# Kernel optimization log

Measured on AMD Instinct MI355X. Metric: run time of the kernel, lower is better.

## Reference

```python
import jax, jax.numpy as jnp
import numpy as np

N_NODES = 100000
N_EDGES = 1600000
NEG_SLOPE = 0.2  # PyG GATConv default


def _glorot(key, shape):
    fan = sum(shape[:2]) if len(shape) > 1 else shape[0] * 2
    s = jnp.sqrt(6.0 / fan)
    return jax.random.uniform(key, shape, jnp.float32, -s, s)


def gat_layer(x, src, dst, edge_attr, W, a_src, a_dst, We, a_e, b, heads, out_ch, concat):
    """Faithful PyG GATConv (add_self_loops=True, fill_value='mean', edge_dim set)."""
    n = x.shape[0]
    # self-loop edge_attr = mean of incoming edge_attr per dst node (0 if none)
    deg = jax.ops.segment_sum(jnp.ones((src.shape[0],), edge_attr.dtype), dst, num_segments=n)
    loop_attr = jax.ops.segment_sum(edge_attr, dst, num_segments=n) / jnp.maximum(deg, 1.0)[:, None]
    loop = jnp.arange(n, dtype=src.dtype)
    src_f = jnp.concatenate([src, loop])
    dst_f = jnp.concatenate([dst, loop])
    ea = jnp.concatenate([edge_attr, loop_attr], axis=0)
    # node transform -> [n, H, C]
    h = (x @ W).reshape(n, heads, out_ch)
    al_src = jnp.sum(h * a_src, axis=-1)  # [n, H]
    al_dst = jnp.sum(h * a_dst, axis=-1)  # [n, H]
    e = (ea @ We).reshape(-1, heads, out_ch)
    al_e = jnp.sum(e * a_e, axis=-1)      # [Ef, H]
    alpha = jax.nn.leaky_relu(al_src[src_f] + al_dst[dst_f] + al_e, negative_slope=NEG_SLOPE)
    # segment softmax over destination nodes (every node has a self loop)
    m = jax.ops.segment_max(alpha, dst_f, num_segments=n)
    ex = jnp.exp(alpha - m[dst_f])
    den = jax.ops.segment_sum(ex, dst_f, num_segments=n)
    att = ex / den[dst_f]                 # [Ef, H]
    out = jax.ops.segment_sum(att[:, :, None] * h[src_f], dst_f, num_segments=n)  # [n, H, C]
    out = out.reshape(n, heads * out_ch) if concat else out.mean(axis=1)
    return out + b


def setup_inputs() -> dict:
    key = jax.random.key(0)
    ks = jax.random.split(key, 20)
    x = jax.random.normal(ks[0], (N_NODES, 5), jnp.float32)
    edge_index = jax.random.randint(ks[1], (2, N_EDGES), 0, N_NODES, jnp.int64)
    edge_attr = jax.random.normal(ks[2], (N_EDGES, 2), jnp.float32)
    # conv1: in=5, out=32, heads=4, concat -> 128
    p = {
        "W1": _glorot(ks[3], (5, 128)), "aS1": _glorot(ks[4], (4, 32)),
        "aD1": _glorot(ks[5], (4, 32)), "We1": _glorot(ks[6], (2, 128)),
        "aE1": _glorot(ks[7], (4, 32)), "b1": jnp.zeros((128,), jnp.float32),
        # conv2: in=128, out=32, heads=2, concat -> 64
        "W2": _glorot(ks[8], (128, 64)), "aS2": _glorot(ks[9], (2, 32)),
        "aD2": _glorot(ks[10], (2, 32)), "We2": _glorot(ks[11], (2, 64)),
        "aE2": _glorot(ks[12], (2, 32)), "b2": jnp.zeros((64,), jnp.float32),
        # conv3: in=64, out=1, heads=1, concat=False
        "W3": _glorot(ks[13], (64, 1)), "aS3": _glorot(ks[14], (1, 1)),
        "aD3": _glorot(ks[15], (1, 1)), "We3": _glorot(ks[16], (2, 1)),
        "aE3": _glorot(ks[17], (1, 1)), "b3": jnp.zeros((1,), jnp.float32),
    }
    return {"x": x, "edge_index": edge_index, "edge_attr": edge_attr, **p}


def reference(x, edge_index, edge_attr,
              W1, aS1, aD1, We1, aE1, b1,
              W2, aS2, aD2, We2, aE2, b2,
              W3, aS3, aD3, We3, aE3, b3):
    src, dst = edge_index[0], edge_index[1]
    h = gat_layer(x, src, dst, edge_attr, W1, aS1, aD1, We1, aE1, b1, 4, 32, True)
    h = jax.nn.elu(h)  # dropout is identity in eval
    h = gat_layer(h, src, dst, edge_attr, W2, aS2, aD2, We2, aE2, b2, 2, 32, True)
    h = jax.nn.elu(h)
    h = gat_layer(h, src, dst, edge_attr, W3, aS3, aD3, We3, aE3, b3, 1, 1, False)
    return jax.nn.sigmoid(h).squeeze(-1)  # [N]
```

## Files before the change

### kernel.cpp

```cpp
#include <hip/hip_runtime.h>
#include <math.h>

#define NN 100000
#define NE 1600000
#define NPB 256
#define NPB_SHIFT 8
#define NB ((NN + NPB - 1) / NPB)
#define NCHUNK 512
#define CH ((NE + NCHUNK - 1) / NCHUNK)
#define LOG2E 1.44269504088896f

__device__ __forceinline__ float lrelu(float x) { return fmaxf(x, 0.2f * x); }
__device__ __forceinline__ float elu1(float x) { return x > 0.f ? x : (__expf(x) - 1.f); }
__device__ __forceinline__ float fexp2(float x) {
#if __has_builtin(__builtin_amdgcn_exp2f)
    return __builtin_amdgcn_exp2f(x);
#else
    return exp2f(x);
#endif
}
__device__ __forceinline__ unsigned bf16rne(float f) {
    unsigned u = __float_as_uint(f);
    return (u + 0x7FFFu + ((u >> 16) & 1u)) >> 16;
}
__device__ __forceinline__ float bf16lo(unsigned u) { return __uint_as_float(u << 16); }
__device__ __forceinline__ float bf16hi(unsigned u) {
    return __uint_as_float(u & 0xFFFF0000u);
}

__global__ void __launch_bounds__(256) k_binA0(const int* __restrict__ dst,
                                               int* __restrict__ bucket_cnt) {
    __shared__ int hist[NB];
    int t = threadIdx.x;
    for (int b = t; b < NB; b += 256) hist[b] = 0;
    __syncthreads();
    int c0 = blockIdx.x * CH, c1 = min(NE, c0 + CH);
    for (int e = c0 + t; e < c1; e += 256) atomicAdd(&hist[dst[e] >> NPB_SHIFT], 1);
    __syncthreads();
    for (int b = t; b < NB; b += 256)
        if (hist[b]) atomicAdd(&bucket_cnt[b], hist[b]);
}

__global__ void __launch_bounds__(512) k_bscan(const int* __restrict__ bucket_cnt,
                                               int* __restrict__ bucket_base,
                                               int* __restrict__ bucket_tail) {
    __shared__ int s[512];
    int t = threadIdx.x;
    int v = (t < NB) ? bucket_cnt[t] : 0;
    s[t] = v;
    __syncthreads();
    for (int off = 1; off < 512; off <<= 1) {
        int x = (t >= off) ? s[t - off] : 0;
        __syncthreads();
        if (t >= off) s[t] += x;
        __syncthreads();
    }
    if (t < NB) {
        int ex = s[t] - v;
        bucket_base[t] = ex;
        bucket_tail[t] = ex;
        if (t == NB - 1) bucket_base[NB] = s[t];
    }
}

__global__ void __launch_bounds__(256) k_binA2(const int* __restrict__ src,
                                               const int* __restrict__ dst,
                                               const float* __restrict__ ea,
                                               int* __restrict__ bucket_tail,
                                               uint2* __restrict__ binned,
                                               unsigned char* __restrict__ dstb) {
    __shared__ int hist[NB], pre[NB], cursor[NB], base_l[NB];
    __shared__ int psum[256];
    __shared__ uint2 lrec[CH];
    __shared__ int lds_d[CH];
    int t = threadIdx.x;
    for (int b = t; b < NB; b += 256) hist[b] = 0;
    __syncthreads();
    int c0 = blockIdx.x * CH, c1 = min(NE, c0 + CH);
    int cnt = c1 - c0;
    for (int i = t; i < cnt; i += 256) atomicAdd(&hist[dst[c0 + i] >> NPB_SHIFT], 1);
    __syncthreads();
    int b0 = t << 1, b1 = b0 + 1;
    int h0 = (b0 < NB) ? hist[b0] : 0;
    int h1 = (b1 < NB) ? hist[b1] : 0;
    psum[t] = h0 + h1;
    __syncthreads();
    for (int off = 1; off < 256; off <<= 1) {
        int x = (t >= off) ? psum[t - off] : 0;
        __syncthreads();
        if (t >= off) psum[t] += x;
        __syncthreads();
    }
    int ex = psum[t] - (h0 + h1);
    if (b0 < NB) { pre[b0] = ex;      cursor[b0] = ex; }
    if (b1 < NB) { pre[b1] = ex + h0; cursor[b1] = ex + h0; }
    for (int b = t; b < NB; b += 256) {
        int h = hist[b];
        if (h) base_l[b] = atomicAdd(&bucket_tail[b], h);
    }
    __syncthreads();
    for (int i = t; i < cnt; i += 256) {
        int e = c0 + i;
        int d = dst[e];
        int bkt = d >> NPB_SHIFT;
        int lpos = atomicAdd(&cursor[bkt], 1);
        unsigned pk = bf16rne(ea[2 * e]) | (bf16rne(ea[2 * e + 1]) << 16);
        lrec[lpos] = make_uint2((unsigned)src[e], pk);
        lds_d[lpos] = d;
    }
    __syncthreads();
    for (int i = t; i < cnt; i += 256) {
        int d = lds_d[i];
        int bkt = d >> NPB_SHIFT;
        int gpos = base_l[bkt] + (i - pre[bkt]);
        binned[gpos] = lrec[i];
        dstb[gpos] = (unsigned char)(d & (NPB - 1));
    }
}

__global__ void __launch_bounds__(256) k_binB(const int* __restrict__ bucket_base,
                                              const uint2* __restrict__ binned,
                                              const unsigned char* __restrict__ dstb,
                                              int* __restrict__ rowptr,
                                              uint2* __restrict__ edges,
                                              float* __restrict__ la) {
    __shared__ int hist[NPB], pre[NPB], cursor[NPB];
    __shared__ float ea0s[NPB], ea1s[NPB];
    int b = blockIdx.x, t = threadIdx.x;
    int bb = bucket_base[b], be = bucket_base[b + 1];
    int nb0 = b << NPB_SHIFT;
    hist[t] = 0;
    ea0s[t] = 0.f;
    ea1s[t] = 0.f;
    __syncthreads();
    for (int e = bb + t; e < be; e += 256) atomicAdd(&hist[dstb[e]], 1);
    __syncthreads();
    int v = hist[t];
    pre[t] = v;
    __syncthreads();
    for (int off = 1; off < 256; off <<= 1) {
        int x = (t >= off) ? pre[t - off] : 0;
        __syncthreads();
        if (t >= off) pre[t] += x;
        __syncthreads();
    }
    int ex = pre[t] - v;
    if (nb0 + t <= NN) rowptr[nb0 + t] = bb + ex;
    cursor[t] = bb + ex;
    __syncthreads();
    for (int e = bb + t; e < be; e += 256) {
        uint2 rec = binned[e];
        unsigned char d = dstb[e];
        int pos = atomicAdd(&cursor[d], 1);
        edges[pos] = rec;
        atomicAdd(&ea0s[d], bf16lo(rec.y));
        atomicAdd(&ea1s[d], bf16hi(rec.y));
    }
    __syncthreads();
    int n = nb0 + t;
    if (n < NN) {
        float dg = fmaxf((float)v, 1.0f);
        la[2 * n] = ea0s[t] / dg;
        la[2 * n + 1] = ea1s[t] / dg;
    }
}

__global__ void k_const(const float* __restrict__ We1, const float* __restrict__ aE1,
                        const float* __restrict__ We2, const float* __restrict__ aE2,
                        const float* __restrict__ We3, const float* __restrict__ aE3,
                        const float* __restrict__ W1, const float* __restrict__ aS1,
                        const float* __restrict__ aD1, float* __restrict__ cbuf) {
    int t = threadIdx.x;
    if (t < 8) {
        int d = t >> 2, hd = t & 3;
        float s = 0.f;
        for (int c = 0; c < 32; c++) s += We1[d * 128 + hd * 32 + c] * aE1[hd * 32 + c];
        cbuf[t] = s * LOG2E;
    } else if (t < 12) {
        int idx = t - 8, d = idx >> 1, hd = idx & 1;
        float s = 0.f;
        for (int c = 0; c < 32; c++) s += We2[d * 64 + hd * 32 + c] * aE2[hd * 32 + c];
        cbuf[t] = s * LOG2E;
    } else if (t < 14) {
        cbuf[t] = We3[t - 12] * aE3[0] * LOG2E;
    } else if (t >= 16 && t < 56) {
        int r = (t - 16) % 20, hd = r / 5, i = r % 5;
        const float* a = (t - 16 < 20) ? aS1 : aD1;
        float s = 0.f;
        for (int c = 0; c < 32; c++) s += W1[i * 128 + hd * 32 + c] * a[hd * 32 + c];
        cbuf[t] = s * LOG2E;
    }
}

__global__ void k_prep1(const float* __restrict__ x, const float* __restrict__ vsd,
                        float4* __restrict__ xp, float4* __restrict__ als1,
                        float4* __restrict__ ald1) {
    int n = blockIdx.x * blockDim.x + threadIdx.x;
    if (n >= NN) return;
    float x0 = x[5 * n], x1 = x[5 * n + 1], x2 = x[5 * n + 2], x3 = x[5 * n + 3],
          x4 = x[5 * n + 4];
    xp[2 * n] = make_float4(x0, x1, x2, x3);
    xp[2 * n + 1] = make_float4(x4, 0.f, 0.f, 0.f);
    float sv[4], dv[4];
#pragma unroll
    for (int hd = 0; hd < 4; hd++) {
        const float* vS = vsd + hd * 5;
        const float* vD = vsd + 20 + hd * 5;
        sv[hd] = x0 * vS[0] + x1 * vS[1] + x2 * vS[2] + x3 * vS[3] + x4 * vS[4];
        dv[hd] = x0 * vD[0] + x1 * vD[1] + x2 * vD[2] + x3 * vD[3] + x4 * vD[4];
    }
    als1[n] = make_float4(sv[0], sv[1], sv[2], sv[3]);
    ald1[n] = make_float4(dv[0], dv[1], dv[2], dv[3]);
}

__global__ void k_agg1(const int* __restrict__ rowptr, const uint2* __restrict__ edges,
                       const float4* __restrict__ xp, const float* __restrict__ als1,
                       const float* __restrict__ ald1, const float* __restrict__ la,
                       const float* __restrict__ me, float* __restrict__ xw) {
    int t = blockIdx.x * blockDim.x + threadIdx.x;
    if (t >= NN * 4) return;
    int n = t >> 2, hd = t & 3;
    float me0 = me[hd], me1 = me[4 + hd];
    float aldn = ald1[t];
    float aself = lrelu(als1[t] + aldn + la[2 * n] * me0 + la[2 * n + 1] * me1);
    int start = rowptr[n], end = rowptr[n + 1];
    float den = 1.f;
    float4 xa = xp[2 * n];
    float xb = xp[2 * n + 1].x;
    float a0 = xa.x, a1 = xa.y, a2 = xa.z, a3 = xa.w, a4 = xb;
    int e = start;
    if ((e & 1) && e < end) {
        uint2 ep = edges[e];
        int s = (int)ep.x;
        float a = lrelu(als1[s * 4 + hd] + aldn + bf16lo(ep.y) * me0 + bf16hi(ep.y) * me1);
        float p = fexp2(a - aself);
        den += p;
        float4 sa = xp[2 * s];
        float sb = xp[2 * s + 1].x;
        a0 += p * sa.x; a1 += p * sa.y; a2 += p * sa.z; a3 += p * sa.w; a4 += p * sb;
        e++;
    }
    for (; e + 1 < end; e += 2) {
        uint4 two = *(const uint4*)(edges + e);
        int s0 = (int)two.x, s1 = (int)two.z;
        unsigned pk0 = two.y, pk1 = two.w;
        float l0 = als1[s0 * 4 + hd];
        float l1 = als1[s1 * 4 + hd];
        float4 sa0 = xp[2 * s0];
        float sb0 = xp[2 * s0 + 1].x;
        float4 sa1 = xp[2 * s1];
        float sb1 = xp[2 * s1 + 1].x;
        float av0 = lrelu(l0 + aldn + bf16lo(pk0) * me0 + bf16hi(pk0) * me1);
        float av1 = lrelu(l1 + aldn + bf16lo(pk1) * me0 + bf16hi(pk1) * me1);
        float p0 = fexp2(av0 - aself);
        float p1 = fexp2(av1 - aself);
        den += p0 + p1;
        a0 += p0 * sa0.x + p1 * sa1.x;
        a1 += p0 * sa0.y + p1 * sa1.y;
        a2 += p0 * sa0.z + p1 * sa1.z;
        a3 += p0 * sa0.w + p1 * sa1.w;
        a4 += p0 * sb0 + p1 * sb1;
    }
    if (e < end) {
        uint2 ep = edges[e];
        int s = (int)ep.x;
        float a = lrelu(als1[s * 4 + hd] + aldn + bf16lo(ep.y) * me0 + bf16hi(ep.y) * me1);
        float p = fexp2(a - aself);
        den += p;
        float4 sa = xp[2 * s];
        float sb = xp[2 * s + 1].x;
        a0 += p * sa.x; a1 += p * sa.y; a2 += p * sa.z; a3 += p * sa.w; a4 += p * sb;
    }
    float r = 1.f / den;
    float* w = xw + (size_t)n * 20 + hd * 5;
    w[0] = a0 * r;
    w[1] = a1 * r;
    w[2] = a2 * r;
    w[3] = a3 * r;
    w[4] = a4 * r;
}

__global__ void __launch_bounds__(256) k_l2trans(
        const float* __restrict__ xw, const float* __restrict__ W1,
        const float* __restrict__ b1, const float* __restrict__ W2,
        const float* __restrict__ aS2, const float* __restrict__ aD2,
        unsigned short* __restrict__ h2q, float* __restrict__ als2,
        float* __restrict__ ald2) {
    __shared__ float wstage[64 * 20];
    __shared__ float sx[64 * 132];
    int nb = blockIdx.x * 64, t = threadIdx.x;
    {
        int base = nb * 20;
        for (int idx = t; idx < 64 * 20; idx += 256) {
            int g = base + idx;
            wstage[idx] = (g < NN * 20) ? xw[g] : 0.f;
        }
    }
    __syncthreads();
    {
        int nl = t >> 2, q = t & 3;
        int node = nb + nl;
        float w[20];
#pragma unroll
        for (int i = 0; i < 20; i++) w[i] = wstage[nl * 20 + i];
#pragma unroll
        for (int k = 0; k < 32; k++) {
            int ch = q + 4 * k;
            int hd = ch >> 5;
            float v = w[hd * 5] * W1[ch] + w[hd * 5 + 1] * W1[128 + ch] +
                      w[hd * 5 + 2] * W1[256 + ch] + w[hd * 5 + 3] * W1[384 + ch] +
                      w[hd * 5 + 4] * W1[512 + ch] + b1[ch];
            sx[nl * 132 + ch] = (node < NN) ? elu1(v) : 0.f;
        }
    }
    __syncthreads();
    int jq = t & 15, ng = t >> 4;
    int j4 = jq * 4;
    float4 acc[4];
#pragma unroll
    for (int p = 0; p < 4; p++) acc[p] = make_float4(0.f, 0.f, 0.f, 0.f);
    for (int ic = 0; ic < 128; ic += 4) {
        float4 s[4];
#pragma unroll
        for (int p = 0; p < 4; p++)
            s[p] = *(const float4*)(sx + (ng * 4 + p) * 132 + ic);
#pragma unroll
        for (int r = 0; r < 4; r++) {
            float4 wv = *(const float4*)(W2 + (ic + r) * 64 + j4);
#pragma unroll
            for (int p = 0; p < 4; p++) {
                float sv = (r == 0) ? s[p].x : (r == 1) ? s[p].y : (r == 2) ? s[p].z : s[p].w;
                acc[p].x += sv * wv.x;
                acc[p].y += sv * wv.y;
                acc[p].z += sv * wv.z;
                acc[p].w += sv * wv.w;
            }
        }
    }
    int hd = jq >> 3;
    float4 a_s = *(const float4*)(aS2 + j4);
    float4 a_d = *(const float4*)(aD2 + j4);
    float pS[4], pD[4];
#pragma unroll
    for (int p = 0; p < 4; p++) {
        pS[p] = acc[p].x * a_s.x + acc[p].y * a_s.y + acc[p].z * a_s.z + acc[p].w * a_s.w;
        pD[p] = acc[p].x * a_d.x + acc[p].y * a_d.y + acc[p].z * a_d.z + acc[p].w * a_d.w;
    }
#pragma unroll
    for (int off = 1; off < 8; off <<= 1) {
#pragma unroll
        for (int p = 0; p < 4; p++) {
            pS[p] += __shfl_xor(pS[p], off);
            pD[p] += __shfl_xor(pD[p], off);
        }
    }
#pragma unroll
    for (int p = 0; p < 4; p++) {
        int node = nb + ng * 4 + p;
        if (node < NN) {
            ushort4 q;
            q.x = (unsigned short)bf16rne(acc[p].x);
            q.y = (unsigned short)bf16rne(acc[p].y);
            q.z = (unsigned short)bf16rne(acc[p].z);
            q.w = (unsigned short)bf16rne(acc[p].w);
            *(ushort4*)(h2q + (size_t)node * 64 + j4) = q;
            if ((jq & 7) == 0) {
                als2[node * 2 + hd] = pS[p] * LOG2E;
                ald2[node * 2 + hd] = pD[p] * LOG2E;
            }
        }
    }
}

__global__ void k_agg2(const int* __restrict__ rowptr, const uint2* __restrict__ edges,
                       const unsigned short* __restrict__ h2q,
                       const float* __restrict__ als2, const float* __restrict__ ald2,
                       const float* __restrict__ la, const float* __restrict__ me,
                       const float* __restrict__ b2, const float* __restrict__ W3,
                       float* __restrict__ h3) {
    int t = blockIdx.x * blockDim.x + threadIdx.x;
    if (t >= NN * 4) return;
    int n = t >> 2, sub = t & 3, hd = sub >> 1, qh = sub & 1;
    int cbase = hd * 32 + qh * 16;
    float me0 = me[hd], me1 = me[2 + hd];
    float aldn = ald2[n * 2 + hd];
    float aself = lrelu(als2[n * 2 + hd] + aldn + la[2 * n] * me0 + la[2 * n + 1] * me1);
    int start = rowptr[n], end = rowptr[n + 1];
    float den = 1.f;
    float acc[16];
    {
        const uint4* hp = (const uint4*)(h2q + (size_t)n * 64 + cbase);
        uint4 u0 = hp[0], u1 = hp[1];
        acc[0] = bf16lo(u0.x); acc[1] = bf16hi(u0.x);
        acc[2] = bf16lo(u0.y); acc[3] = bf16hi(u0.y);
        acc[4] = bf16lo(u0.z); acc[5] = bf16hi(u0.z);
        acc[6] = bf16lo(u0.w); acc[7] = bf16hi(u0.w);
        acc[8] = bf16lo(u1.x); acc[9] = bf16hi(u1.x);
        acc[10] = bf16lo(u1.y); acc[11] = bf16hi(u1.y);
        acc[12] = bf16lo(u1.z); acc[13] = bf16hi(u1.z);
        acc[14] = bf16lo(u1.w); acc[15] = bf16hi(u1.w);
    }
    int e = start;
    if ((e & 1) && e < end) {
        uint2 ep = edges[e];
        int s = (int)ep.x;
        float a = lrelu(als2[s * 2 + hd] + aldn + bf16lo(ep.y) * me0 + bf16hi(ep.y) * me1);
        float p = fexp2(a - aself);
        den += p;
        const uint4* sp = (const uint4*)(h2q + (size_t)s * 64 + cbase);
        uint4 u0 = sp[0], u1 = sp[1];
        acc[0] += p * bf16lo(u0.x); acc[1] += p * bf16hi(u0.x);
        acc[2] += p * bf16lo(u0.y); acc[3] += p * bf16hi(u0.y);
        acc[4] += p * bf16lo(u0.z); acc[5] += p * bf16hi(u0.z);
        acc[6] += p * bf16lo(u0.w); acc[7] += p * bf16hi(u0.w);
        acc[8] += p * bf16lo(u1.x); acc[9] += p * bf16hi(u1.x);
        acc[10] += p * bf16lo(u1.y); acc[11] += p * bf16hi(u1.y);
        acc[12] += p * bf16lo(u1.z); acc[13] += p * bf16hi(u1.z);
        acc[14] += p * bf16lo(u1.w); acc[15] += p * bf16hi(u1.w);
        e++;
    }
    for (; e + 1 < end; e += 2) {
        uint4 two = *(const uint4*)(edges + e);
        int s0 = (int)two.x, s1 = (int)two.z;
        unsigned pk0 = two.y, pk1 = two.w;
        float l0 = als2[s0 * 2 + hd];
        float l1 = als2[s1 * 2 + hd];
        const uint4* sp0 = (const uint4*)(h2q + (size_t)s0 * 64 + cbase);
        const uint4* sp1 = (const uint4*)(h2q + (size_t)s1 * 64 + cbase);
        uint4 u00 = sp0[0], u01 = sp0[1];
        uint4 u10 = sp1[0], u11 = sp1[1];
        float av0 = lrelu(l0 + aldn + bf16lo(pk0) * me0 + bf16hi(pk0) * me1);
        float av1 = lrelu(l1 + aldn + bf16lo(pk1) * me0 + bf16hi(pk1) * me1);
        float p0 = fexp2(av0 - aself);
        float p1 = fexp2(av1 - aself);
        den += p0 + p1;
        acc[0] += p0 * bf16lo(u00.x) + p1 * bf16lo(u10.x);
        acc[1] += p0 * bf16hi(u00.x) + p1 * bf16hi(u10.x);
        acc[2] += p0 * bf16lo(u00.y) + p1 * bf16lo(u10.y);
        acc[3] += p0 * bf16hi(u00.y) + p1 * bf16hi(u10.y);
        acc[4] += p0 * bf16lo(u00.z) + p1 * bf16lo(u10.z);
        acc[5] += p0 * bf16hi(u00.z) + p1 * bf16hi(u10.z);
        acc[6] += p0 * bf16lo(u00.w) + p1 * bf16lo(u10.w);
        acc[7] += p0 * bf16hi(u00.w) + p1 * bf16hi(u10.w);
        acc[8] += p0 * bf16lo(u01.x) + p1 * bf16lo(u11.x);
        acc[9] += p0 * bf16hi(u01.x) + p1 * bf16hi(u11.x);
        acc[10] += p0 * bf16lo(u01.y) + p1 * bf16lo(u11.y);
        acc[11] += p0 * bf16hi(u01.y) + p1 * bf16hi(u11.y);
        acc[12] += p0 * bf16lo(u01.z) + p1 * bf16lo(u11.z);
        acc[13] += p0 * bf16hi(u01.z) + p1 * bf16hi(u11.z);
        acc[14] += p0 * bf16lo(u01.w) + p1 * bf16lo(u11.w);
        acc[15] += p0 * bf16hi(u01.w) + p1 * bf16hi(u11.w);
    }
    if (e < end) {
        uint2 ep = edges[e];
        int s = (int)ep.x;
        float a = lrelu(als2[s * 2 + hd] + aldn + bf16lo(ep.y) * me0 + bf16hi(ep.y) * me1);
        float p = fexp2(a - aself);
        den += p;
        const uint4* sp = (const uint4*)(h2q + (size_t)s * 64 + cbase);
        uint4 u0 = sp[0], u1 = sp[1];
        acc[0] += p * bf16lo(u0.x); acc[1] += p * bf16hi(u0.x);
        acc[2] += p * bf16lo(u0.y); acc[3] += p * bf16hi(u0.y);
        acc[4] += p * bf16lo(u0.z); acc[5] += p * bf16hi(u0.z);
        acc[6] += p * bf16lo(u0.w); acc[7] += p * bf16hi(u0.w);
        acc[8] += p * bf16lo(u1.x); acc[9] += p * bf16hi(u1.x);
        acc[10] += p * bf16lo(u1.y); acc[11] += p * bf16hi(u1.y);
        acc[12] += p * bf16lo(u1.z); acc[13] += p * bf16hi(u1.z);
        acc[14] += p * bf16lo(u1.w); acc[15] += p * bf16hi(u1.w);
    }
    float r = 1.f / den;
    float part = 0.f;
#pragma unroll
    for (int c = 0; c < 16; c++) {
        float v = elu1(acc[c] * r + b2[cbase + c]);
        part += v * W3[cbase + c];
    }
    part += __shfl_xor(part, 1);
    part += __shfl_xor(part, 2);
    if (sub == 0) h3[n] = part;
}

__global__ void k_agg3(const int* __restrict__ rowptr, const uint2* __restrict__ edges,
                       const float* __restrict__ h, const float* __restrict__ aS3,
                       const float* __restrict__ aD3, const float* __restrict__ la,
                       const float* __restrict__ me, const float* __restrict__ b,
                       float* __restrict__ out) {
    int n = (blockIdx.x * blockDim.x + threadIdx.x) >> 6;
    if (n >= NN) return;
    int lane = threadIdx.x & 63;
    float me0 = me[0], me1 = me[1];
    float aSs = aS3[0] * LOG2E, aDs = aD3[0] * LOG2E;
    float hn = h[n];
    float ald_n = hn * aDs;
    float aself = lrelu(hn * aSs + ald_n + la[2 * n] * me0 + la[2 * n + 1] * me1);
    int start = rowptr[n], end = rowptr[n + 1];
    float den = 0.f, num = 0.f;
    for (int e = start + lane; e < end; e += 64) {
        uint2 ep = edges[e];
        int s = (int)ep.x;
        float hv = h[s];
        float a = lrelu(hv * aSs + ald_n + bf16lo(ep.y) * me0 + bf16hi(ep.y) * me1);
        float p = fexp2(a - aself);
        den += p;
        num += p * hv;
    }
#pragma unroll
    for (int off = 32; off > 0; off >>= 1) {
        den += __shfl_xor(den, off);
        num += __shfl_xor(num, off);
    }
    if (lane == 0) {
        den += 1.f;
        num += hn;
        float v = num / den + b[0];
        out[n] = 1.f / (1.f + __expf(-v));
    }
}

extern "C" void kernel_launch(void* const* d_in, const int* in_sizes, int n_in,
                              void* d_out, int out_size, void* d_ws, size_t ws_size,
                              hipStream_t stream) {
    const float* x   = (const float*)d_in[0];
    const int*   ei  = (const int*)d_in[1];
    const float* ea  = (const float*)d_in[2];
    const float* W1  = (const float*)d_in[3];
    const float* aS1 = (const float*)d_in[4];
    const float* aD1 = (const float*)d_in[5];
    const float* We1 = (const float*)d_in[6];
    const float* aE1 = (const float*)d_in[7];
    const float* b1  = (const float*)d_in[8];
    const float* W2  = (const float*)d_in[9];
    const float* aS2 = (const float*)d_in[10];
    const float* aD2 = (const float*)d_in[11];
    const float* We2 = (const float*)d_in[12];
    const float* aE2 = (const float*)d_in[13];
    const float* b2  = (const float*)d_in[14];
    const float* W3  = (const float*)d_in[15];
    const float* aS3 = (const float*)d_in[16];
    const float* aD3 = (const float*)d_in[17];
    const float* We3 = (const float*)d_in[18];
    const float* aE3 = (const float*)d_in[19];
    const float* b3  = (const float*)d_in[20];

    const int* srcv = ei;
    const int* dstv = ei + NE;

    char* basep = (char*)d_ws;
    size_t off = 0;
    auto alloc = [&](size_t nbytes) -> void* {
        void* p = basep + off;
        off += (nbytes + 255) & ~(size_t)255;
        return p;
    };
    int*    bucket_cnt  = (int*)alloc((size_t)(NB + 1) * 4);
    int*    bucket_base = (int*)alloc((size_t)(NB + 1) * 4);
    int*    bucket_tail = (int*)alloc((size_t)(NB + 1) * 4);
    int*    rowptr      = (int*)alloc((size_t)(NN + 1) * 4);
    uint2*  binned      = (uint2*)alloc((size_t)NE * 8);
    unsigned char* dstb = (unsigned char*)alloc((size_t)NE);
    uint2*  edges       = (uint2*)alloc((size_t)NE * 8);
    float*  la          = (float*)alloc((size_t)NN * 8);
    float*  cbuf        = (float*)alloc(256);
    float4* xp          = (float4*)alloc((size_t)NN * 32);
    float4* als1        = (float4*)alloc((size_t)NN * 16);
    float4* ald1        = (float4*)alloc((size_t)NN * 16);
    float*  xw          = (float*)alloc((size_t)NN * 80);
    unsigned short* h2q = (unsigned short*)alloc((size_t)NN * 128);
    float*  als2        = (float*)alloc((size_t)NN * 8);
    float*  ald2        = (float*)alloc((size_t)NN * 8);
    float*  h3          = (float*)alloc((size_t)NN * 4);
    (void)ws_size; (void)in_sizes; (void)n_in; (void)out_size;

    float* me1 = cbuf;
    float* me2 = cbuf + 8;
    float* me3 = cbuf + 12;
    float* vsd = cbuf + 16;

    auto cdiv = [](long long a, long long b) { return (int)((a + b - 1) / b); };
    const int BS = 256;

    hipMemsetAsync(bucket_cnt, 0, (size_t)(NB + 1) * 4, stream);
    k_binA0<<<NCHUNK, 256, 0, stream>>>(dstv, bucket_cnt);
    k_bscan<<<1, 512, 0, stream>>>(bucket_cnt, bucket_base, bucket_tail);
    k_binA2<<<NCHUNK, 256, 0, stream>>>(srcv, dstv, ea, bucket_tail, binned, dstb);
    k_binB<<<NB, 256, 0, stream>>>(bucket_base, binned, dstb, rowptr, edges, la);

    k_const<<<1, 64, 0, stream>>>(We1, aE1, We2, aE2, We3, aE3, W1, aS1, aD1, cbuf);

    k_prep1<<<cdiv(NN, BS), BS, 0, stream>>>(x, vsd, xp, als1, ald1);
    k_agg1<<<cdiv((long long)NN * 4, BS), BS, 0, stream>>>(rowptr, edges, xp,
                                                           (const float*)als1,
                                                           (const float*)ald1, la, me1, xw);

    k_l2trans<<<cdiv(NN, 64), 256, 0, stream>>>(xw, W1, b1, W2, aS2, aD2, h2q, als2, ald2);
    k_agg2<<<cdiv((long long)NN * 4, BS), BS, 0, stream>>>(rowptr, edges, h2q, als2, ald2,
                                                           la, me2, b2, W3, h3);

    k_agg3<<<cdiv(NN, 4), 256, 0, stream>>>(rowptr, edges, h3, aS3, aD3, la, me3,
                                            b3, (float*)d_out);
}
```

Before: 339.1 us.

## Compute layer-2 transform with split-bf16 MFMA instead of FP32 FMA loops

Replaces the scalar FP32 128x64 matmul in the layer-2 transform kernel with bf16 MFMA 16x16x32 instructions. It recovers near-FP32 accuracy by splitting each operand into hi/lo bf16 parts (three MFMAs per tile). A new small kernel pre-transposes and splits W2 once, and blocks shrink to 32 nodes and 128 threads. The shared-memory layout is rearranged to feed MFMA fragments directly. The cost is an extra launch and a slight precision change, and the code assumes NN is a multiple of 32, since the bounds checks were removed.

```diff
diff --git a/kernel.cpp b/kernel.cpp
--- a/kernel.cpp
+++ b/kernel.cpp
@@ -10,6 +10,9 @@
 #define CH ((NE + NCHUNK - 1) / NCHUNK)
 #define LOG2E 1.44269504088896f
 
+typedef __attribute__((ext_vector_type(8))) short short8v;
+typedef __attribute__((ext_vector_type(4))) float f32x4;
+
 __device__ __forceinline__ float lrelu(float x) { return fmaxf(x, 0.2f * x); }
 __device__ __forceinline__ float elu1(float x) { return x > 0.f ? x : (__expf(x) - 1.f); }
 __device__ __forceinline__ float fexp2(float x) {
@@ -26,6 +29,13 @@
 __device__ __forceinline__ float bf16lo(unsigned u) { return __uint_as_float(u << 16); }
 __device__ __forceinline__ float bf16hi(unsigned u) {
     return __uint_as_float(u & 0xFFFF0000u);
+}
+__device__ __forceinline__ void split2(float x0, float x1, unsigned& hp, unsigned& lp) {
+    unsigned h0 = bf16rne(x0), h1 = bf16rne(x1);
+    float r0 = x0 - __uint_as_float(h0 << 16);
+    float r1 = x1 - __uint_as_float(h1 << 16);
+    hp = h0 | (h1 << 16);
+    lp = bf16rne(r0) | (bf16rne(r1) << 16);
 }
 
 __global__ void __launch_bounds__(256) k_binA0(const int* __restrict__ dst,
@@ -190,6 +200,19 @@
         for (int c = 0; c < 32; c++) s += W1[i * 128 + hd * 32 + c] * a[hd * 32 + c];
         cbuf[t] = s * LOG2E;
     }
+}
+
+__global__ void k_w2t(const float* __restrict__ W2, unsigned short* __restrict__ W2th,
+                      unsigned short* __restrict__ W2tl) {
+    int i = blockIdx.x * 256 + threadIdx.x;
+    if (i >= 64 * 128) return;
+    int c = i >> 7, k = i & 127;
+    float v = W2[k * 64 + c];
+    unsigned h = bf16rne(v);
+    float hf = __uint_as_float(h << 16);
+    unsigned lo = bf16rne(v - hf);
+    W2th[c * 128 + k] = (unsigned short)h;
+    W2tl[c * 128 + k] = (unsigned short)lo;
 }
 
 __global__ void k_prep1(const float* __restrict__ x, const float* __restrict__ vsd,
@@ -280,93 +303,128 @@
     w[4] = a4 * r;
 }
 
-__global__ void __launch_bounds__(256) k_l2trans(
+__global__ void __launch_bounds__(128) k_l2trans(
         const float* __restrict__ xw, const float* __restrict__ W1,
-        const float* __restrict__ b1, const float* __restrict__ W2,
+        const float* __restrict__ b1, const unsigned short* __restrict__ W2th,
+        const unsigned short* __restrict__ W2tl,
         const float* __restrict__ aS2, const float* __restrict__ aD2,
         unsigned short* __restrict__ h2q, float* __restrict__ als2,
         float* __restrict__ ald2) {
-    __shared__ float wstage[64 * 20];
-    __shared__ float sx[64 * 132];
-    int nb = blockIdx.x * 64, t = threadIdx.x;
+    __shared__ float wstage[32 * 20];
+    __shared__ unsigned short Ahi[4096];
+    __shared__ unsigned short Alo[4096];
+    int nb = blockIdx.x * 32, t = threadIdx.x;
     {
         int base = nb * 20;
-        for (int idx = t; idx < 64 * 20; idx += 256) {
-            int g = base + idx;
-            wstage[idx] = (g < NN * 20) ? xw[g] : 0.f;
+        for (int idx = t; idx < 32 * 20; idx += 128) wstage[idx] = xw[base + idx];
+    }
+    __syncthreads();
+    {
+        int nl = t >> 2, g = t & 3;
+        int w = nl >> 4, row = nl & 15;
+#pragma unroll
+        for (int kt = 0; kt < 4; ++kt) {
+            int ch0 = kt * 32 + g * 8;
+            float4 va = *(const float4*)(b1 + ch0);
+            float4 vb = *(const float4*)(b1 + ch0 + 4);
+            const float* wp = wstage + nl * 20 + kt * 5;
+#pragma unroll
+            for (int i = 0; i < 5; ++i) {
+                float wi = wp[i];
+                float4 A = *(const float4*)(W1 + i * 128 + ch0);
+                float4 B = *(const float4*)(W1 + i * 128 + ch0 + 4);
+                va.x += wi * A.x; va.y += wi * A.y; va.z += wi * A.z; va.w += wi * A.w;
+                vb.x += wi * B.x; vb.y += wi * B.y; vb.z += wi * B.z; vb.w += wi * B.w;
+            }
+            unsigned hp0, hp1, hp2, hp3, lp0, lp1, lp2, lp3;
+            split2(elu1(va.x), elu1(va.y), hp0, lp0);
+            split2(elu1(va.z), elu1(va.w), hp1, lp1);
+            split2(elu1(vb.x), elu1(vb.y), hp2, lp2);
+            split2(elu1(vb.z), elu1(vb.w), hp3, lp3);
+            int cidx = (((w * 4 + kt) * 64) + g * 16 + row) * 8;
+            *(uint4*)(Ahi + cidx) = make_uint4(hp0, hp1, hp2, hp3);
+            *(uint4*)(Alo + cidx) = make_uint4(lp0, lp1, lp2, lp3);
         }
     }
-    __syncthreads();
+    int l = t & 63, w = t >> 6;
+    int g = l >> 4, row16 = l & 15;
+    f32x4 acc0 = {0.f, 0.f, 0.f, 0.f}, acc1 = acc0, acc2 = acc0, acc3 = acc0;
+    int w4 = w * 4;
+#pragma unroll
+    for (int kt = 0; kt < 4; ++kt) {
+        int abase = ((w4 + kt) * 64 + l) * 8;
+        short8v ah = *(const short8v*)(Ahi + abase);
+        short8v al = *(const short8v*)(Alo + abase);
+        int kb = kt * 32 + g * 8;
+        {
+            short8v bh = *(const short8v*)(W2th + row16 * 128 + kb);
+            short8v bl = *(const short8v*)(W2tl + row16 * 128 + kb);
+            acc0 = __builtin_amdgcn_mfma_f32_16x16x32_bf16(ah, bh, acc0, 0, 0, 0);
+            acc0 = __builtin_amdgcn_mfma_f32_16x16x32_bf16(al, bh, acc0, 0, 0, 0);
+            acc0 = __builtin_amdgcn_mfma_f32_16x16x32_bf16(ah, bl, acc0, 0, 0, 0);
+        }
+        {
+            short8v bh = *(const short8v*)(W2th + (16 + row16) * 128 + kb);
+            short8v bl = *(const short8v*)(W2tl + (16 + row16) * 128 + kb);
+            acc1 = __builtin_amdgcn_mfma_f32_16x16x32_bf16(ah, bh, acc1, 0, 0, 0);
+            acc1 = __builtin_amdgcn_mfma_f32_16x16x32_bf16(al, bh, acc1, 0, 0, 0);
+            acc1 = __builtin_amdgcn_mfma_f32_16x16x32_bf16(ah, bl, acc1, 0, 0, 0);
+        }
+        {
+            short8v bh = *(const short8v*)(W2th + (32 + row16) * 128 + kb);
+            short8v bl = *(const short8v*)(W2tl + (32 + row16) * 128 + kb);
+            acc2 = __builtin_amdgcn_mfma_f32_16x16x32_bf16(ah, bh, acc2, 0, 0, 0);
+            acc2 = __builtin_amdgcn_mfma_f32_16x16x32_bf16(al, bh, acc2, 0, 0, 0);
+            acc2 = __builtin_amdgcn_mfma_f32_16x16x32_bf16(ah, bl, acc2, 0, 0, 0);
+        }
+        {
+            short8v bh = *(const short8v*)(W2th + (48 + row16) * 128 + kb);
+            short8v bl = *(const short8v*)(W2tl + (48 + row16) * 128 + kb);
+            acc3 = __builtin_amdgcn_mfma_f32_16x16x32_bf16(ah, bh, acc3, 0, 0, 0);
+            acc3 = __builtin_amdgcn_mfma_f32_16x16x32_bf16(al, bh, acc3, 0, 0, 0);
+            acc3 = __builtin_amdgcn_mfma_f32_16x16x32_bf16(ah, bl, acc3, 0, 0, 0);
+        }
+    }
     {
-        int nl = t >> 2, q = t & 3;
-        int node = nb + nl;
-        float w[20];
-#pragma unroll
-        for (int i = 0; i < 20; i++) w[i] = wstage[nl * 20 + i];
-#pragma unroll
-        for (int k = 0; k < 32; k++) {
-            int ch = q + 4 * k;
-            int hd = ch >> 5;
-            float v = w[hd * 5] * W1[ch] + w[hd * 5 + 1] * W1[128 + ch] +
-                      w[hd * 5 + 2] * W1[256 + ch] + w[hd * 5 + 3] * W1[384 + ch] +
-                      w[hd * 5 + 4] * W1[512 + ch] + b1[ch];
-            sx[nl * 132 + ch] = (node < NN) ? elu1(v) : 0.f;
-        }
-    }
-    __syncthreads();
-    int jq = t & 15, ng = t >> 4;
-    int j4 = jq * 4;
-    float4 acc[4];
-#pragma unroll
-    for (int p = 0; p < 4; p++) acc[p] = make_float4(0.f, 0.f, 0.f, 0.f);
-    for (int ic = 0; ic < 128; ic += 4) {
-        float4 s[4];
-#pragma unroll
-        for (int p = 0; p < 4; p++)
-            s[p] = *(const float4*)(sx + (ng * 4 + p) * 132 + ic);
-#pragma unroll
-        for (int r = 0; r < 4; r++) {
-            float4 wv = *(const float4*)(W2 + (ic + r) * 64 + j4);
-#pragma unroll
-            for (int p = 0; p < 4; p++) {
-                float sv = (r == 0) ? s[p].x : (r == 1) ? s[p].y : (r == 2) ? s[p].z : s[p].w;
-                acc[p].x += sv * wv.x;
-                acc[p].y += sv * wv.y;
-                acc[p].z += sv * wv.z;
-                acc[p].w += sv * wv.w;
+        int nodeb = nb + w * 16 + g * 4;
+#pragma unroll
+        for (int nt = 0; nt < 4; ++nt) {
+            f32x4 A = (nt == 0) ? acc0 : (nt == 1) ? acc1 : (nt == 2) ? acc2 : acc3;
+#pragma unroll
+            for (int r = 0; r < 4; ++r) {
+                float v = A[r];
+                float u = __shfl_xor(v, 1);
+                if (!(l & 1)) {
+                    unsigned pk = bf16rne(v) | (bf16rne(u) << 16);
+                    int node = nodeb + r;
+                    int ch = nt * 16 + row16;
+                    *(unsigned*)(h2q + (size_t)node * 64 + ch) = pk;
+                }
             }
         }
-    }
-    int hd = jq >> 3;
-    float4 a_s = *(const float4*)(aS2 + j4);
-    float4 a_d = *(const float4*)(aD2 + j4);
-    float pS[4], pD[4];
-#pragma unroll
-    for (int p = 0; p < 4; p++) {
-        pS[p] = acc[p].x * a_s.x + acc[p].y * a_s.y + acc[p].z * a_s.z + acc[p].w * a_s.w;
-        pD[p] = acc[p].x * a_d.x + acc[p].y * a_d.y + acc[p].z * a_d.z + acc[p].w * a_d.w;
-    }
-#pragma unroll
-    for (int off = 1; off < 8; off <<= 1) {
-#pragma unroll
-        for (int p = 0; p < 4; p++) {
-            pS[p] += __shfl_xor(pS[p], off);
-            pD[p] += __shfl_xor(pD[p], off);
-        }
-    }
-#pragma unroll
-    for (int p = 0; p < 4; p++) {
-        int node = nb + ng * 4 + p;
-        if (node < NN) {
-            ushort4 q;
-            q.x = (unsigned short)bf16rne(acc[p].x);
-            q.y = (unsigned short)bf16rne(acc[p].y);
-            q.z = (unsigned short)bf16rne(acc[p].z);
-            q.w = (unsigned short)bf16rne(acc[p].w);
-            *(ushort4*)(h2q + (size_t)node * 64 + j4) = q;
-            if ((jq & 7) == 0) {
-                als2[node * 2 + hd] = pS[p] * LOG2E;
-                ald2[node * 2 + hd] = pD[p] * LOG2E;
+        float aSv0 = aS2[row16], aSv1 = aS2[16 + row16];
+        float aSv2 = aS2[32 + row16], aSv3 = aS2[48 + row16];
+        float aDv0 = aD2[row16], aDv1 = aD2[16 + row16];
+        float aDv2 = aD2[32 + row16], aDv3 = aD2[48 + row16];
+#pragma unroll
+        for (int r = 0; r < 4; ++r) {
+            float pS0 = acc0[r] * aSv0 + acc1[r] * aSv1;
+            float pS1 = acc2[r] * aSv2 + acc3[r] * aSv3;
+            float pD0 = acc0[r] * aDv0 + acc1[r] * aDv1;
+            float pD1 = acc2[r] * aDv2 + acc3[r] * aDv3;
+#pragma unroll
+            for (int off = 1; off < 16; off <<= 1) {
+                pS0 += __shfl_xor(pS0, off);
+                pS1 += __shfl_xor(pS1, off);
+                pD0 += __shfl_xor(pD0, off);
+                pD1 += __shfl_xor(pD1, off);
+            }
+            if (row16 == 0) {
+                int node = nodeb + r;
+                als2[node * 2 + 0] = pS0 * LOG2E;
+                als2[node * 2 + 1] = pS1 * LOG2E;
+                ald2[node * 2 + 0] = pD0 * LOG2E;
+                ald2[node * 2 + 1] = pD1 * LOG2E;
             }
         }
     }
@@ -569,6 +627,8 @@
     float*  als2        = (float*)alloc((size_t)NN * 8);
     float*  ald2        = (float*)alloc((size_t)NN * 8);
     float*  h3          = (float*)alloc((size_t)NN * 4);
+    unsigned short* W2th = (unsigned short*)alloc(64 * 128 * 2);
+    unsigned short* W2tl = (unsigned short*)alloc(64 * 128 * 2);
     (void)ws_size; (void)in_sizes; (void)n_in; (void)out_size;
 
     float* me1 = cbuf;
@@ -586,13 +646,15 @@
     k_binB<<<NB, 256, 0, stream>>>(bucket_base, binned, dstb, rowptr, edges, la);
 
     k_const<<<1, 64, 0, stream>>>(We1, aE1, We2, aE2, We3, aE3, W1, aS1, aD1, cbuf);
+    k_w2t<<<32, 256, 0, stream>>>(W2, W2th, W2tl);
 
     k_prep1<<<cdiv(NN, BS), BS, 0, stream>>>(x, vsd, xp, als1, ald1);
     k_agg1<<<cdiv((long long)NN * 4, BS), BS, 0, stream>>>(rowptr, edges, xp,
                                                            (const float*)als1,
                                                            (const float*)ald1, la, me1, xw);
 
-    k_l2trans<<<cdiv(NN, 64), 256, 0, stream>>>(xw, W1, b1, W2, aS2, aD2, h2q, als2, ald2);
+    k_l2trans<<<cdiv(NN, 32), 128, 0, stream>>>(xw, W1, b1, W2th, W2tl, aS2, aD2,
+                                                h2q, als2, ald2);
     k_agg2<<<cdiv((long long)NN * 4, BS), BS, 0, stream>>>(rowptr, edges, h2q, als2, ald2,
                                                            la, me2, b2, W3, h3);
 
```

New measurement: 328.9 us. 1.03x faster.
